# Kernel optimization log

Measured on AMD Instinct MI355X. Metric: run time of the kernel, lower is better.

Reference implementation:

```python
import jax, jax.numpy as jnp
import numpy as np

N = 20000          # nodes
E = 320000         # directed edges (self-loops added in reference)
F_IN = 128         # input node features
HEADS = 8
HID = 64           # per-head hidden channels
G = 64             # graphs in the batch
NUM_CLASSES = 10
NEG_SLOPE = 0.2    # PyG GATConv LeakyReLU slope


def _gat_layer(x, src, dst, W, a_src, a_dst, bias, n_nodes):
    """PyG-style GATConv: messages flow src->dst, softmax over incoming edges."""
    H, C = a_src.shape
    h = (x @ W).reshape(n_nodes, H, C)                     # [N,H,C]
    asrc = jnp.einsum('nhc,hc->nh', h, a_src)              # [N,H]
    adst = jnp.einsum('nhc,hc->nh', h, a_dst)              # [N,H]
    e = jax.nn.leaky_relu(asrc[src] + adst[dst], NEG_SLOPE)  # [Etot,H]
    emax = jax.ops.segment_max(e, dst, num_segments=n_nodes)  # [N,H]
    ee = jnp.exp(e - emax[dst])
    denom = jax.ops.segment_sum(ee, dst, num_segments=n_nodes)
    alpha = ee / (denom[dst] + 1e-16)                      # [Etot,H]
    out = jax.ops.segment_sum(h[src] * alpha[:, :, None], dst, num_segments=n_nodes)
    return out.reshape(n_nodes, H * C) + bias


def setup_inputs() -> dict:
    key = jax.random.key(0)
    ks = jax.random.split(key, 10)
    x = jax.random.normal(ks[0], (N, F_IN), jnp.float32)
    edge_index = jax.random.randint(ks[1], (2, E), 0, N, jnp.int32)
    batch = jnp.sort(jax.random.randint(ks[2], (N,), 0, G, jnp.int32))
    # layer 1: F_IN -> HEADS*HID (concat)
    W1 = jax.random.normal(ks[3], (F_IN, HEADS * HID), jnp.float32) / np.float32(np.sqrt(F_IN))
    a_src1 = jax.random.normal(ks[4], (HEADS, HID), jnp.float32) / np.float32(np.sqrt(HID))
    a_dst1 = jax.random.normal(ks[5], (HEADS, HID), jnp.float32) / np.float32(np.sqrt(HID))
    b1 = jnp.zeros((HEADS * HID,), jnp.float32)
    # layer 2: HEADS*HID -> NUM_CLASSES (1 head)
    W2 = jax.random.normal(ks[6], (HEADS * HID, NUM_CLASSES), jnp.float32) / np.float32(np.sqrt(HEADS * HID))
    a_src2 = jax.random.normal(ks[7], (1, NUM_CLASSES), jnp.float32) / np.float32(np.sqrt(NUM_CLASSES))
    a_dst2 = jax.random.normal(ks[8], (1, NUM_CLASSES), jnp.float32) / np.float32(np.sqrt(NUM_CLASSES))
    b2 = jnp.zeros((NUM_CLASSES,), jnp.float32)
    return {"x": x, "edge_index": edge_index, "batch": batch,
            "W1": W1, "a_src1": a_src1, "a_dst1": a_dst1, "b1": b1,
            "W2": W2, "a_src2": a_src2, "a_dst2": a_dst2, "b2": b2}


def reference(x, edge_index, batch, W1, a_src1, a_dst1, b1, W2, a_src2, a_dst2, b2):
    n = x.shape[0]
    loop = jnp.arange(n, dtype=edge_index.dtype)   # add_self_loops=True (PyG default)
    src = jnp.concatenate([edge_index[0], loop])
    dst = jnp.concatenate([edge_index[1], loop])
    h = jax.nn.elu(_gat_layer(x, src, dst, W1, a_src1, a_dst1, b1, n))
    h = _gat_layer(h, src, dst, W2, a_src2, a_dst2, b2, n)
    # PowerMeanAggregation with default p=1.0 == mean pooling per graph
    sums = jax.ops.segment_sum(h, batch, num_segments=G)                    # [G,NC]
    counts = jax.ops.segment_sum(jnp.ones((n, 1), h.dtype), batch, num_segments=G)
    return sums / jnp.maximum(counts, 1.0)
```

## Files before the change

kernel.cpp:

```cpp
#include <hip/hip_runtime.h>
#include <hip/hip_bf16.h>

typedef unsigned short ushort_t;
typedef unsigned int uint_t;
typedef unsigned char uchar_t;

typedef __attribute__((ext_vector_type(8))) short bf16x8;
typedef __attribute__((ext_vector_type(4))) float f32x4;
typedef __attribute__((ext_vector_type(2))) float f32x2;

__device__ __forceinline__ float bf2f(ushort_t u) {
    union { uint_t i; float f; } v; v.i = ((uint_t)u) << 16; return v.f;
}
__device__ __forceinline__ ushort_t f2bf(float f) {
    __hip_bfloat16 h = __float2bfloat16(f);
    ushort_t u; __builtin_memcpy(&u, &h, 2); return u;
}
__device__ __forceinline__ float leaky(float v) { return (v > 0.f) ? v : 0.2f * v; }

#define PO_AS1 0
#define PO_AD1 512
#define PO_B1  1024
#define PO_W2  1536
#define PO_AS2 6656
#define PO_AD2 6666
#define PO_B2  6676
#define PTOT   6686

__device__ __forceinline__ bool detect_fp32_local(const ushort_t* __restrict__ xa) {
    __shared__ int cnt;
    if (threadIdx.x == 0) cnt = 0;
    __syncthreads();
    int bad = 0;
    for (int i = threadIdx.x; i < 4096; i += 256) {
        float v = bf2f(xa[i]);
        if (!(fabsf(v) < 1e4f)) bad++;
    }
    if (bad) atomicAdd(&cnt, bad);
    __syncthreads();
    return cnt >= 16;
}

__global__ __launch_bounds__(256) void k_prep(const void* __restrict__ x,
                                              const void* __restrict__ W1,
                                              const void* as1, const void* ad1,
                                              const void* b1, const void* W2,
                                              const void* as2, const void* ad2,
                                              const void* b2,
                                              ushort_t* __restrict__ W1t,
                                              float* __restrict__ prm,
                                              float* __restrict__ vab,
                                              int* __restrict__ deg,
                                              float* __restrict__ gacc,
                                              int* __restrict__ flag, int N) {
    int b = blockIdx.x, t = threadIdx.x;
    if (b < 283) {
        bool isf = detect_fp32_local((const ushort_t*)x);
        if (b == 0 && t == 0) *flag = isf ? 1 : 0;
        if (b < 256) {
            int idx = b * 256 + t;
            int n = idx & 511, k = idx >> 9;
            float v = isf ? ((const float*)W1)[k * 512 + n]
                          : bf2f(((const ushort_t*)W1)[k * 512 + n]);
            W1t[n * 128 + k] = f2bf(v);
        } else {
            int i = (b - 256) * 256 + t;
            if (i < PTOT) {
                const void* src; int off;
                if (i < 512)       { src = as1; off = i; }
                else if (i < 1024) { src = ad1; off = i - 512; }
                else if (i < 1536) { src = b1;  off = i - 1024; }
                else if (i < 6656) { src = W2;  off = i - 1536; }
                else if (i < 6666) { src = as2; off = i - 6656; }
                else if (i < 6676) { src = ad2; off = i - 6666; }
                else               { src = b2;  off = i - 6676; }
                prm[i] = isf ? ((const float*)src)[off] : bf2f(((const ushort_t*)src)[off]);
            }
        }
    } else if (b < 362) {
        int i = (b - 283) * 256 + t;
        if (i < N) deg[i] = 0;
    } else if (b == 362) {
        for (int i = t; i < 704; i += 256) gacc[i] = 0.f;
    } else {
        bool isf = detect_fp32_local((const ushort_t*)x);
        int idx = (b - 363) * 256 + t;
        int k = idx >> 4, q = idx & 15;
        int h = q & 7;
        const void* av = (q < 8) ? as1 : ad1;
        float s = 0.f;
        for (int c = 0; c < 64; ++c) {
            float wv = isf ? ((const float*)W1)[k * 512 + h * 64 + c]
                           : bf2f(((const ushort_t*)W1)[k * 512 + h * 64 + c]);
            float aval = isf ? ((const float*)av)[h * 64 + c]
                             : bf2f(((const ushort_t*)av)[h * 64 + c]);
            s += wv * aval;
        }
        vab[k * 16 + q] = s;
    }
}

__global__ __launch_bounds__(256) void k_logits_hist(const void* __restrict__ xraw,
                                                     const float* __restrict__ vab,
                                                     const int* __restrict__ ei,
                                                     const int* __restrict__ flag,
                                                     uchar_t* __restrict__ xq,
                                                     float* __restrict__ asrcf,
                                                     float* __restrict__ adstf,
                                                     int* __restrict__ deg,
                                                     int E, int Etot) {
    int b = blockIdx.x, t = threadIdx.x;
    if (b >= 1250) {
        int e = (b - 1250) * 256 + t;
        if (e < Etot) {
            int dst = (e < E) ? ei[E + e] : (e - E);
            atomicAdd(&deg[dst], 1);
        }
        return;
    }
    bool isf = (*flag != 0);
    int n = b * 16 + (t >> 4);
    int l = t & 15;
    int ch0 = l * 8;
    float xf[8];
    if (isf) {
        const float4* x4 = (const float4*)xraw + (size_t)n * 32 + l * 2;
        float4 f0 = x4[0], f1 = x4[1];
        xf[0] = f0.x; xf[1] = f0.y; xf[2] = f0.z; xf[3] = f0.w;
        xf[4] = f1.x; xf[5] = f1.y; xf[6] = f1.z; xf[7] = f1.w;
    } else {
        uint4 u = ((const uint4*)((const ushort_t*)xraw + (size_t)n * 128))[l];
        xf[0] = bf2f(u.x & 0xffff); xf[1] = bf2f(u.x >> 16);
        xf[2] = bf2f(u.y & 0xffff); xf[3] = bf2f(u.y >> 16);
        xf[4] = bf2f(u.z & 0xffff); xf[5] = bf2f(u.z >> 16);
        xf[6] = bf2f(u.w & 0xffff); xf[7] = bf2f(u.w >> 16);
    }
    uint_t u0 = (uint_t)__builtin_amdgcn_cvt_pk_fp8_f32(xf[0], xf[1], 0, false);
    u0 = (uint_t)__builtin_amdgcn_cvt_pk_fp8_f32(xf[2], xf[3], (int)u0, true);
    uint_t u1 = (uint_t)__builtin_amdgcn_cvt_pk_fp8_f32(xf[4], xf[5], 0, false);
    u1 = (uint_t)__builtin_amdgcn_cvt_pk_fp8_f32(xf[6], xf[7], (int)u1, true);
    uint2 st; st.x = u0; st.y = u1;
    *((uint2*)(xq + (size_t)n * 128) + l) = st;
    float ps[8], pd[8];
#pragma unroll
    for (int h = 0; h < 8; ++h) { ps[h] = 0.f; pd[h] = 0.f; }
#pragma unroll
    for (int j = 0; j < 8; ++j) {
        const float4* vr = (const float4*)&vab[(ch0 + j) * 16];
        float4 va0 = vr[0], va1 = vr[1], vb0 = vr[2], vb1 = vr[3];
        float xv = xf[j];
        ps[0] += xv * va0.x; ps[1] += xv * va0.y; ps[2] += xv * va0.z; ps[3] += xv * va0.w;
        ps[4] += xv * va1.x; ps[5] += xv * va1.y; ps[6] += xv * va1.z; ps[7] += xv * va1.w;
        pd[0] += xv * vb0.x; pd[1] += xv * vb0.y; pd[2] += xv * vb0.z; pd[3] += xv * vb0.w;
        pd[4] += xv * vb1.x; pd[5] += xv * vb1.y; pd[6] += xv * vb1.z; pd[7] += xv * vb1.w;
    }
#pragma unroll
    for (int off = 1; off <= 8; off <<= 1) {
#pragma unroll
        for (int h = 0; h < 8; ++h) {
            ps[h] += __shfl_xor(ps[h], off, 64);
            pd[h] += __shfl_xor(pd[h], off, 64);
        }
    }
    if (l == 0) {
#pragma unroll
        for (int h = 0; h < 8; ++h) {
            asrcf[n * 8 + h] = ps[h];
            adstf[n * 8 + h] = pd[h];
        }
    }
}

__global__ __launch_bounds__(256) void k_scan(const int* __restrict__ deg,
                                              int* __restrict__ rowptr,
                                              int* __restrict__ cursor, int N) {
    int b = blockIdx.x, t = threadIdx.x;
    int lane = t & 63, wv = t >> 6;
    __shared__ int ws[4], wt[4];
    __shared__ int sbase;
    int limit = b * 256;
    int p0 = 0, p1 = 0, p2 = 0, p3 = 0;
    int i = t;
    for (; i + 768 < limit; i += 1024) {
        p0 += deg[i]; p1 += deg[i + 256]; p2 += deg[i + 512]; p3 += deg[i + 768];
    }
    for (; i < limit; i += 256) p0 += deg[i];
    int partial = (p0 + p1) + (p2 + p3);
#pragma unroll
    for (int off = 32; off; off >>= 1) partial += __shfl_xor(partial, off, 64);
    if (lane == 0) ws[wv] = partial;
    __syncthreads();
    if (t == 0) sbase = ws[0] + ws[1] + ws[2] + ws[3];
    __syncthreads();
    int base = sbase;
    i = limit + t;
    int v = (i < N) ? deg[i] : 0;
    int inc = v;
#pragma unroll
    for (int off = 1; off < 64; off <<= 1) {
        int u = __shfl_up(inc, off, 64);
        if (lane >= off) inc += u;
    }
    if (lane == 63) wt[wv] = inc;
    __syncthreads();
    int woff = 0;
    for (int w = 0; w < 4; ++w) if (w < wv) woff += wt[w];
    int excl = base + woff + inc - v;
    if (i < N) { rowptr[i + 1] = excl + v; cursor[i] = excl; }
    if (i == 0) rowptr[0] = 0;
}

__global__ __launch_bounds__(256) void k_scatter(const int* __restrict__ ei,
                                                 int* __restrict__ cursor,
                                                 const float* __restrict__ asrcf,
                                                 const float* __restrict__ adstf,
                                                 int* __restrict__ csr_src,
                                                 float* __restrict__ wcsr,
                                                 int E, int Etot) {
    int e = blockIdx.x * 256 + threadIdx.x;
    if (e >= Etot) return;
    int src, dst;
    if (e < E) { src = ei[e]; dst = ei[E + e]; } else { src = dst = e - E; }
    int pos = atomicAdd(&cursor[dst], 1);
    csr_src[pos] = src;
    const float4* ap = (const float4*)&asrcf[(size_t)src * 8];
    const float4* bp = (const float4*)&adstf[(size_t)dst * 8];
    float4 a0 = ap[0], a1 = ap[1];
    float4 b0 = bp[0], b1 = bp[1];
    float4 w0, w1;
    w0.x = __expf(leaky(a0.x + b0.x));
    w0.y = __expf(leaky(a0.y + b0.y));
    w0.z = __expf(leaky(a0.z + b0.z));
    w0.w = __expf(leaky(a0.w + b0.w));
    w1.x = __expf(leaky(a1.x + b1.x));
    w1.y = __expf(leaky(a1.y + b1.y));
    w1.z = __expf(leaky(a1.z + b1.z));
    w1.w = __expf(leaky(a1.w + b1.w));
    float4* wp = (float4*)&wcsr[(size_t)pos * 8];
    wp[0] = w0; wp[1] = w1;
}

__global__ __launch_bounds__(256) void k_aggx(const uchar_t* __restrict__ xq,
                                              const int* __restrict__ rowptr,
                                              const int* __restrict__ csr_src,
                                              const float* __restrict__ wcsr,
                                              ushort_t* __restrict__ agg) {
    int wid = threadIdx.x >> 6;
    int ni = wid >> 1;
    int half = wid & 1;
    int n = blockIdx.x * 2 + ni;
    int lane = threadIdx.x & 63;
    int start = rowptr[n], end = rowptr[n + 1];
    int deg = end - start;
    int mid = (deg + 1) >> 1;
    int es = start + (half ? mid : 0);
    int ee = half ? end : (start + mid);
    float acc[16];
    float den[8];
#pragma unroll
    for (int i = 0; i < 16; ++i) acc[i] = 0.f;
#pragma unroll
    for (int h = 0; h < 8; ++h) den[h] = 0.f;
    for (int base = es; base < ee; base += 64) {
        int m = min(64, ee - base);
        int sIdx = csr_src[base + min(lane, m - 1)];
        for (int g = 0; g < m; g += 4) {
            int s[4]; float4 wA[4], wB[4]; ushort_t xv[4];
#pragma unroll
            for (int j = 0; j < 4; ++j)
                s[j] = __shfl(sIdx, min(g + j, m - 1), 64);
#pragma unroll
            for (int j = 0; j < 4; ++j) {
                const float4* wp = (const float4*)&wcsr[(size_t)(base + g + j) * 8];
                wA[j] = wp[0]; wB[j] = wp[1];
            }
#pragma unroll
            for (int j = 0; j < 4; ++j)
                xv[j] = *(const ushort_t*)&xq[(size_t)s[j] * 128 + lane * 2];
#pragma unroll
            for (int j = 0; j < 4; ++j) {
                float msk = (g + j < m) ? 1.f : 0.f;
                f32x2 q = __builtin_amdgcn_cvt_pk_f32_fp8((int)xv[j], false);
                float w0 = wA[j].x * msk, w1 = wA[j].y * msk, w2 = wA[j].z * msk, w3 = wA[j].w * msk;
                float w4 = wB[j].x * msk, w5 = wB[j].y * msk, w6 = wB[j].z * msk, w7 = wB[j].w * msk;
                den[0] += w0; acc[0]  += w0 * q.x; acc[1]  += w0 * q.y;
                den[1] += w1; acc[2]  += w1 * q.x; acc[3]  += w1 * q.y;
                den[2] += w2; acc[4]  += w2 * q.x; acc[5]  += w2 * q.y;
                den[3] += w3; acc[6]  += w3 * q.x; acc[7]  += w3 * q.y;
                den[4] += w4; acc[8]  += w4 * q.x; acc[9]  += w4 * q.y;
                den[5] += w5; acc[10] += w5 * q.x; acc[11] += w5 * q.y;
                den[6] += w6; acc[12] += w6 * q.x; acc[13] += w6 * q.y;
                den[7] += w7; acc[14] += w7 * q.x; acc[15] += w7 * q.y;
            }
        }
    }
    __shared__ float sac[2][64][17];
    __shared__ float sdn[2][8];
    if (half) {
#pragma unroll
        for (int i = 0; i < 16; ++i) sac[ni][lane][i] = acc[i];
        if (lane == 0) {
#pragma unroll
            for (int h = 0; h < 8; ++h) sdn[ni][h] = den[h];
        }
    }
    __syncthreads();
    if (half) return;
#pragma unroll
    for (int i = 0; i < 16; ++i) acc[i] += sac[ni][lane][i];
    uint_t* arow = (uint_t*)&agg[(size_t)n * 1024];
#pragma unroll
    for (int h = 0; h < 8; ++h) {
        float inv = 1.f / (den[h] + sdn[ni][h] + 1e-16f);
        uint_t u = (uint_t)f2bf(acc[2 * h] * inv) | ((uint_t)f2bf(acc[2 * h + 1] * inv) << 16);
        arow[h * 64 + lane] = u;
    }
}

__global__ __launch_bounds__(256) void k_gemm2(const ushort_t* __restrict__ agg,
                                               const ushort_t* __restrict__ w1t,
                                               const float* __restrict__ prm,
                                               ushort_t* __restrict__ h2,
                                               float* __restrict__ asrc2f,
                                               float* __restrict__ adst2f) {
    __shared__ ushort_t sA[16 * 1040];
    int b = blockIdx.x, t = threadIdx.x;
    int m0 = b * 16;
    {
        const uint4* gsrc = (const uint4*)(agg + (size_t)m0 * 1024);
        for (int i = t; i < 2048; i += 256) {
            int row = i >> 7, part = i & 127;
            ((uint4*)sA)[row * 130 + part] = gsrc[i];
        }
    }
    __syncthreads();
    int wave = t >> 6, lane = t & 63;
    int mr = lane & 15, quad = lane >> 4;
    int n0 = wave * 128;
    f32x4 acc[8];
#pragma unroll
    for (int ct = 0; ct < 8; ++ct) acc[ct] = {0.f, 0.f, 0.f, 0.f};
#pragma unroll
    for (int kk = 0; kk < 4; ++kk) {
        bf16x8 a0 = *reinterpret_cast<const bf16x8*>(
            &sA[mr * 1040 + (wave * 2) * 128 + quad * 8 + kk * 32]);
        bf16x8 a1 = *reinterpret_cast<const bf16x8*>(
            &sA[mr * 1040 + (wave * 2 + 1) * 128 + quad * 8 + kk * 32]);
#pragma unroll
        for (int ct = 0; ct < 8; ++ct) {
            bf16x8 bb = *reinterpret_cast<const bf16x8*>(
                &w1t[(size_t)(n0 + ct * 16 + mr) * 128 + quad * 8 + kk * 32]);
            acc[ct] = __builtin_amdgcn_mfma_f32_16x16x32_bf16(ct < 4 ? a0 : a1, bb, acc[ct], 0, 0, 0);
        }
    }
    __syncthreads();
    ushort_t* h1s = sA;
    int col = lane & 15;
#pragma unroll
    for (int ct = 0; ct < 8; ++ct) {
        int abscol = n0 + ct * 16 + col;
        float bb1 = prm[PO_B1 + abscol];
#pragma unroll
        for (int r = 0; r < 4; ++r) {
            float v = acc[ct][r] + bb1;
            v = (v > 0.f) ? v : expm1f(v);
            h1s[(quad * 4 + r) * 512 + abscol] = f2bf(v);
        }
    }
    __syncthreads();
    int cb = lane * 8;
    for (int mm = 0; mm < 4; ++mm) {
        int m = wave * 4 + mm;
        int n = m0 + m;
        bf16x8 hv = *reinterpret_cast<const bf16x8*>(&h1s[m * 512 + cb]);
        float p2[10];
#pragma unroll
        for (int c = 0; c < 10; ++c) p2[c] = 0.f;
#pragma unroll
        for (int j = 0; j < 8; ++j) {
            float rv = bf2f((ushort_t)hv[j]);
            const float2* wrow = reinterpret_cast<const float2*>(&prm[PO_W2 + (cb + j) * 10]);
            float2 w01 = wrow[0], w23 = wrow[1], w45 = wrow[2], w67 = wrow[3], w89 = wrow[4];
            p2[0] += rv * w01.x; p2[1] += rv * w01.y;
            p2[2] += rv * w23.x; p2[3] += rv * w23.y;
            p2[4] += rv * w45.x; p2[5] += rv * w45.y;
            p2[6] += rv * w67.x; p2[7] += rv * w67.y;
            p2[8] += rv * w89.x; p2[9] += rv * w89.y;
        }
#pragma unroll
        for (int c = 0; c < 10; ++c)
#pragma unroll
            for (int off = 32; off; off >>= 1)
                p2[c] += __shfl_xor(p2[c], off, 64);
        if (lane == 0) {
            float as = 0.f, ad = 0.f;
#pragma unroll
            for (int c = 0; c < 10; ++c) {
                h2[(size_t)n * 16 + c] = f2bf(p2[c]);
                as += p2[c] * prm[PO_AS2 + c];
                ad += p2[c] * prm[PO_AD2 + c];
            }
            asrc2f[n] = as; adst2f[n] = ad;
        }
    }
}

__global__ __launch_bounds__(256) void k_agg2(const ushort_t* __restrict__ h2,
                                              const float* __restrict__ asrc2f,
                                              const float* __restrict__ adst2f,
                                              const int* __restrict__ rowptr,
                                              const int* __restrict__ csr_src,
                                              const float* __restrict__ prm,
                                              const int* __restrict__ batch,
                                              float* __restrict__ gacc,
                                              float* __restrict__ gcnt) {
    int t = threadIdx.x;
    int grp = t >> 4, l = t & 15;
    int n = blockIdx.x * 16 + grp;
    int start = rowptr[n], end = rowptr[n + 1];
    float adn = adst2f[n];
    float den = 0.f;
    float oc[10];
#pragma unroll
    for (int c = 0; c < 10; ++c) oc[c] = 0.f;
    for (int e = start + l; e < end; e += 16) {
        int s = csr_src[e];
        float lo = asrc2f[s];
        const uint_t* hp = (const uint_t*)(h2 + (size_t)s * 16);
        uint4 ha = *(const uint4*)hp;
        uint_t hb = hp[4];
        float ee = __expf(leaky(lo + adn));
        den += ee;
        oc[0] += ee * bf2f(ha.x & 0xffff); oc[1] += ee * bf2f(ha.x >> 16);
        oc[2] += ee * bf2f(ha.y & 0xffff); oc[3] += ee * bf2f(ha.y >> 16);
        oc[4] += ee * bf2f(ha.z & 0xffff); oc[5] += ee * bf2f(ha.z >> 16);
        oc[6] += ee * bf2f(ha.w & 0xffff); oc[7] += ee * bf2f(ha.w >> 16);
        oc[8] += ee * bf2f(hb & 0xffff);   oc[9] += ee * bf2f(hb >> 16);
    }
#pragma unroll
    for (int off = 8; off; off >>= 1) {
        den += __shfl_xor(den, off, 64);
#pragma unroll
        for (int c = 0; c < 10; ++c) oc[c] += __shfl_xor(oc[c], off, 64);
    }
    __shared__ float sres[16][12];
    __shared__ int sg[16];
    if (l == 0) {
        float invd = 1.f / (den + 1e-16f);
#pragma unroll
        for (int c = 0; c < 10; ++c) sres[grp][c] = oc[c] * invd + prm[PO_B2 + c];
        sres[grp][10] = 1.f;
        sg[grp] = batch[n];
    }
    __syncthreads();
    if (t < 11) {
        int c = t;
        float run = sres[0][c]; int g = sg[0];
        for (int k = 1; k < 16; ++k) {
            if (sg[k] != g) {
                atomicAdd(c < 10 ? &gacc[g * 10 + c] : &gcnt[g], run);
                g = sg[k]; run = 0.f;
            }
            run += sres[k][c];
        }
        atomicAdd(c < 10 ? &gacc[g * 10 + c] : &gcnt[g], run);
    }
}

__global__ void k_final(const float* __restrict__ gacc,
                        const float* __restrict__ gcnt,
                        const int* __restrict__ flag,
                        void* __restrict__ dout) {
    int g = threadIdx.x;
    if (g >= 64) return;
    bool isf = (*flag != 0);
    float cnt = fmaxf(gcnt[g], 1.f);
    for (int c = 0; c < 10; ++c) {
        float r = gacc[g * 10 + c] / cnt;
        if (isf) ((float*)dout)[g * 10 + c] = r;
        else     ((ushort_t*)dout)[g * 10 + c] = f2bf(r);
    }
}

extern "C" void kernel_launch(void* const* d_in, const int* in_sizes, int n_in,
                              void* d_out, int out_size, void* d_ws, size_t ws_size,
                              hipStream_t stream) {
    const void* x   = d_in[0];
    const int* ei   = (const int*)d_in[1];
    const int* batch= (const int*)d_in[2];
    const void* W1  = d_in[3];
    const void* as1 = d_in[4];
    const void* ad1 = d_in[5];
    const void* b1  = d_in[6];
    const void* W2  = d_in[7];
    const void* as2 = d_in[8];
    const void* ad2 = d_in[9];
    const void* b2  = d_in[10];

    constexpr int N = 20000, E = 320000, Etot = E + N;
    constexpr int histBlocks = (Etot + 255) / 256;

    char* p = (char*)d_ws;
    auto alloc = [&](size_t bytes) {
        char* r = p; p += (bytes + 255) & ~(size_t)255; return r;
    };
    int* flag       = (int*)alloc(256);
    float* prm      = (float*)alloc((size_t)PTOT * 4);
    float* vab      = (float*)alloc(2048 * 4);
    ushort_t* w1t   = (ushort_t*)alloc(512 * 128 * 2);
    uchar_t* xq     = (uchar_t*)alloc((size_t)N * 128);
    float* asrc1f   = (float*)alloc((size_t)N * 8 * 4);
    float* adst1f   = (float*)alloc((size_t)N * 8 * 4);
    float* asrc2f   = (float*)alloc((size_t)N * 4);
    float* adst2f   = (float*)alloc((size_t)N * 4);
    ushort_t* h2    = (ushort_t*)alloc((size_t)N * 16 * 2);
    float* gacc     = (float*)alloc((size_t)(64 * 10 + 64) * 4);
    int* deg        = (int*)alloc((size_t)N * 4);
    int* rowptr     = (int*)alloc((size_t)(N + 1) * 4);
    int* cursor     = (int*)alloc((size_t)N * 4);
    int* csr_src    = (int*)alloc((size_t)(Etot + 64) * 4);
    float* wcsr     = (float*)alloc(((size_t)Etot * 8 + 128) * 4);
    ushort_t* agg   = (ushort_t*)alloc((size_t)N * 1024 * 2);
    float* gcnt     = gacc + 640;

    k_prep<<<371, 256, 0, stream>>>(x, W1, as1, ad1, b1, W2, as2, ad2, b2,
                                    w1t, prm, vab, deg, gacc, flag, N);
    k_logits_hist<<<1250 + histBlocks, 256, 0, stream>>>(x, vab, ei, flag, xq,
                                                         asrc1f, adst1f, deg, E, Etot);
    k_scan<<<(N + 255) / 256, 256, 0, stream>>>(deg, rowptr, cursor, N);
    k_scatter<<<histBlocks, 256, 0, stream>>>(ei, cursor, asrc1f, adst1f,
                                              csr_src, wcsr, E, Etot);
    k_aggx<<<N / 2, 256, 0, stream>>>(xq, rowptr, csr_src, wcsr, agg);
    k_gemm2<<<1250, 256, 0, stream>>>(agg, w1t, prm, h2, asrc2f, adst2f);
    k_agg2<<<N / 16, 256, 0, stream>>>(h2, asrc2f, adst2f, rowptr, csr_src, prm,
                                       batch, gacc, gcnt);
    k_final<<<1, 64, 0, stream>>>(gacc, gcnt, flag, d_out);
}
```

Baseline: 256.6 us.

## Fuse layer-1 aggregation into GEMM kernel and fold final mean into agg2

The layer-1 neighbor aggregation now writes each block's 16 aggregated rows straight into shared memory and feeds the MFMA GEMM directly. This removes the global bf16 agg buffer (20000x1024) and one kernel launch. The final mean-pooling kernel is folded into agg2 using a last-block-done atomic counter. The trade-off is less aggregation parallelism: one wave handles 4 nodes serially with no split-half reduction, and 1250 blocks replace 10000, so latency hiding for the gather may be worse.

```diff
diff --git a/kernel.cpp b/kernel.cpp
--- a/kernel.cpp
+++ b/kernel.cpp
@@ -81,7 +81,7 @@
         int i = (b - 283) * 256 + t;
         if (i < N) deg[i] = 0;
     } else if (b == 362) {
-        for (int i = t; i < 704; i += 256) gacc[i] = 0.f;
+        for (int i = t; i < 768; i += 256) gacc[i] = 0.f;
     } else {
         bool isf = detect_fp32_local((const ushort_t*)x);
         int idx = (b - 363) * 256 + t;
@@ -240,106 +240,75 @@
     wp[0] = w0; wp[1] = w1;
 }
 
-__global__ __launch_bounds__(256) void k_aggx(const uchar_t* __restrict__ xq,
-                                              const int* __restrict__ rowptr,
-                                              const int* __restrict__ csr_src,
-                                              const float* __restrict__ wcsr,
-                                              ushort_t* __restrict__ agg) {
-    int wid = threadIdx.x >> 6;
-    int ni = wid >> 1;
-    int half = wid & 1;
-    int n = blockIdx.x * 2 + ni;
-    int lane = threadIdx.x & 63;
-    int start = rowptr[n], end = rowptr[n + 1];
-    int deg = end - start;
-    int mid = (deg + 1) >> 1;
-    int es = start + (half ? mid : 0);
-    int ee = half ? end : (start + mid);
-    float acc[16];
-    float den[8];
-#pragma unroll
-    for (int i = 0; i < 16; ++i) acc[i] = 0.f;
-#pragma unroll
-    for (int h = 0; h < 8; ++h) den[h] = 0.f;
-    for (int base = es; base < ee; base += 64) {
-        int m = min(64, ee - base);
-        int sIdx = csr_src[base + min(lane, m - 1)];
-        for (int g = 0; g < m; g += 4) {
-            int s[4]; float4 wA[4], wB[4]; ushort_t xv[4];
-#pragma unroll
-            for (int j = 0; j < 4; ++j)
-                s[j] = __shfl(sIdx, min(g + j, m - 1), 64);
-#pragma unroll
-            for (int j = 0; j < 4; ++j) {
-                const float4* wp = (const float4*)&wcsr[(size_t)(base + g + j) * 8];
-                wA[j] = wp[0]; wB[j] = wp[1];
-            }
-#pragma unroll
-            for (int j = 0; j < 4; ++j)
-                xv[j] = *(const ushort_t*)&xq[(size_t)s[j] * 128 + lane * 2];
-#pragma unroll
-            for (int j = 0; j < 4; ++j) {
-                float msk = (g + j < m) ? 1.f : 0.f;
-                f32x2 q = __builtin_amdgcn_cvt_pk_f32_fp8((int)xv[j], false);
-                float w0 = wA[j].x * msk, w1 = wA[j].y * msk, w2 = wA[j].z * msk, w3 = wA[j].w * msk;
-                float w4 = wB[j].x * msk, w5 = wB[j].y * msk, w6 = wB[j].z * msk, w7 = wB[j].w * msk;
-                den[0] += w0; acc[0]  += w0 * q.x; acc[1]  += w0 * q.y;
-                den[1] += w1; acc[2]  += w1 * q.x; acc[3]  += w1 * q.y;
-                den[2] += w2; acc[4]  += w2 * q.x; acc[5]  += w2 * q.y;
-                den[3] += w3; acc[6]  += w3 * q.x; acc[7]  += w3 * q.y;
-                den[4] += w4; acc[8]  += w4 * q.x; acc[9]  += w4 * q.y;
-                den[5] += w5; acc[10] += w5 * q.x; acc[11] += w5 * q.y;
-                den[6] += w6; acc[12] += w6 * q.x; acc[13] += w6 * q.y;
-                den[7] += w7; acc[14] += w7 * q.x; acc[15] += w7 * q.y;
-            }
-        }
-    }
-    __shared__ float sac[2][64][17];
-    __shared__ float sdn[2][8];
-    if (half) {
-#pragma unroll
-        for (int i = 0; i < 16; ++i) sac[ni][lane][i] = acc[i];
-        if (lane == 0) {
-#pragma unroll
-            for (int h = 0; h < 8; ++h) sdn[ni][h] = den[h];
-        }
-    }
-    __syncthreads();
-    if (half) return;
-#pragma unroll
-    for (int i = 0; i < 16; ++i) acc[i] += sac[ni][lane][i];
-    uint_t* arow = (uint_t*)&agg[(size_t)n * 1024];
-#pragma unroll
-    for (int h = 0; h < 8; ++h) {
-        float inv = 1.f / (den[h] + sdn[ni][h] + 1e-16f);
-        uint_t u = (uint_t)f2bf(acc[2 * h] * inv) | ((uint_t)f2bf(acc[2 * h + 1] * inv) << 16);
-        arow[h * 64 + lane] = u;
-    }
-}
-
-__global__ __launch_bounds__(256) void k_gemm2(const ushort_t* __restrict__ agg,
-                                               const ushort_t* __restrict__ w1t,
-                                               const float* __restrict__ prm,
-                                               ushort_t* __restrict__ h2,
-                                               float* __restrict__ asrc2f,
-                                               float* __restrict__ adst2f) {
+__global__ __launch_bounds__(256) void k_aggfused(const uchar_t* __restrict__ xq,
+                                                  const int* __restrict__ rowptr,
+                                                  const int* __restrict__ csr_src,
+                                                  const float* __restrict__ wcsr,
+                                                  const ushort_t* __restrict__ w1t,
+                                                  const float* __restrict__ prm,
+                                                  ushort_t* __restrict__ h2,
+                                                  float* __restrict__ asrc2f,
+                                                  float* __restrict__ adst2f) {
     __shared__ ushort_t sA[16 * 1040];
     int b = blockIdx.x, t = threadIdx.x;
     int m0 = b * 16;
-    {
-        const uint4* gsrc = (const uint4*)(agg + (size_t)m0 * 1024);
-        for (int i = t; i < 2048; i += 256) {
-            int row = i >> 7, part = i & 127;
-            ((uint4*)sA)[row * 130 + part] = gsrc[i];
-        }
-    }
-    __syncthreads();
     int wave = t >> 6, lane = t & 63;
+    for (int mm = 0; mm < 4; ++mm) {
+        int mloc = wave * 4 + mm;
+        int n = m0 + mloc;
+        int start = rowptr[n], end = rowptr[n + 1];
+        float acc[16];
+        float den[8];
+#pragma unroll
+        for (int i = 0; i < 16; ++i) acc[i] = 0.f;
+#pragma unroll
+        for (int h = 0; h < 8; ++h) den[h] = 0.f;
+        for (int base = start; base < end; base += 64) {
+            int mcap = min(64, end - base);
+            int sIdx = csr_src[base + min(lane, mcap - 1)];
+            for (int g = 0; g < mcap; g += 4) {
+                int s[4]; float4 wA[4], wB[4]; ushort_t xv[4];
+#pragma unroll
+                for (int j = 0; j < 4; ++j)
+                    s[j] = __shfl(sIdx, min(g + j, mcap - 1), 64);
+#pragma unroll
+                for (int j = 0; j < 4; ++j) {
+                    const float4* wp = (const float4*)&wcsr[(size_t)(base + min(g + j, mcap - 1)) * 8];
+                    wA[j] = wp[0]; wB[j] = wp[1];
+                }
+#pragma unroll
+                for (int j = 0; j < 4; ++j)
+                    xv[j] = *(const ushort_t*)&xq[(size_t)s[j] * 128 + lane * 2];
+#pragma unroll
+                for (int j = 0; j < 4; ++j) {
+                    float msk = (g + j < mcap) ? 1.f : 0.f;
+                    f32x2 q = __builtin_amdgcn_cvt_pk_f32_fp8((int)xv[j], false);
+                    float w0 = wA[j].x * msk, w1 = wA[j].y * msk, w2 = wA[j].z * msk, w3 = wA[j].w * msk;
+                    float w4 = wB[j].x * msk, w5 = wB[j].y * msk, w6 = wB[j].z * msk, w7 = wB[j].w * msk;
+                    den[0] += w0; acc[0]  += w0 * q.x; acc[1]  += w0 * q.y;
+                    den[1] += w1; acc[2]  += w1 * q.x; acc[3]  += w1 * q.y;
+                    den[2] += w2; acc[4]  += w2 * q.x; acc[5]  += w2 * q.y;
+                    den[3] += w3; acc[6]  += w3 * q.x; acc[7]  += w3 * q.y;
+                    den[4] += w4; acc[8]  += w4 * q.x; acc[9]  += w4 * q.y;
+                    den[5] += w5; acc[10] += w5 * q.x; acc[11] += w5 * q.y;
+                    den[6] += w6; acc[12] += w6 * q.x; acc[13] += w6 * q.y;
+                    den[7] += w7; acc[14] += w7 * q.x; acc[15] += w7 * q.y;
+                }
+            }
+        }
+#pragma unroll
+        for (int h = 0; h < 8; ++h) {
+            float inv = 1.f / (den[h] + 1e-16f);
+            uint_t u = (uint_t)f2bf(acc[2 * h] * inv) | ((uint_t)f2bf(acc[2 * h + 1] * inv) << 16);
+            *(uint_t*)&sA[mloc * 1040 + h * 128 + 2 * lane] = u;
+        }
+    }
+    __syncthreads();
     int mr = lane & 15, quad = lane >> 4;
     int n0 = wave * 128;
-    f32x4 acc[8];
-#pragma unroll
-    for (int ct = 0; ct < 8; ++ct) acc[ct] = {0.f, 0.f, 0.f, 0.f};
+    f32x4 acc2[8];
+#pragma unroll
+    for (int ct = 0; ct < 8; ++ct) acc2[ct] = {0.f, 0.f, 0.f, 0.f};
 #pragma unroll
     for (int kk = 0; kk < 4; ++kk) {
         bf16x8 a0 = *reinterpret_cast<const bf16x8*>(
@@ -350,7 +319,7 @@
         for (int ct = 0; ct < 8; ++ct) {
             bf16x8 bb = *reinterpret_cast<const bf16x8*>(
                 &w1t[(size_t)(n0 + ct * 16 + mr) * 128 + quad * 8 + kk * 32]);
-            acc[ct] = __builtin_amdgcn_mfma_f32_16x16x32_bf16(ct < 4 ? a0 : a1, bb, acc[ct], 0, 0, 0);
+            acc2[ct] = __builtin_amdgcn_mfma_f32_16x16x32_bf16(ct < 4 ? a0 : a1, bb, acc2[ct], 0, 0, 0);
         }
     }
     __syncthreads();
@@ -362,7 +331,7 @@
         float bb1 = prm[PO_B1 + abscol];
 #pragma unroll
         for (int r = 0; r < 4; ++r) {
-            float v = acc[ct][r] + bb1;
+            float v = acc2[ct][r] + bb1;
             v = (v > 0.f) ? v : expm1f(v);
             h1s[(quad * 4 + r) * 512 + abscol] = f2bf(v);
         }
@@ -405,15 +374,18 @@
     }
 }
 
-__global__ __launch_bounds__(256) void k_agg2(const ushort_t* __restrict__ h2,
-                                              const float* __restrict__ asrc2f,
-                                              const float* __restrict__ adst2f,
-                                              const int* __restrict__ rowptr,
-                                              const int* __restrict__ csr_src,
-                                              const float* __restrict__ prm,
-                                              const int* __restrict__ batch,
-                                              float* __restrict__ gacc,
-                                              float* __restrict__ gcnt) {
+__global__ __launch_bounds__(256) void k_agg2f(const ushort_t* __restrict__ h2,
+                                               const float* __restrict__ asrc2f,
+                                               const float* __restrict__ adst2f,
+                                               const int* __restrict__ rowptr,
+                                               const int* __restrict__ csr_src,
+                                               const float* __restrict__ prm,
+                                               const int* __restrict__ batch,
+                                               float* __restrict__ gacc,
+                                               float* __restrict__ gcnt,
+                                               int* __restrict__ donecnt,
+                                               const int* __restrict__ flag,
+                                               void* __restrict__ dout) {
     int t = threadIdx.x;
     int grp = t >> 4, l = t & 15;
     int n = blockIdx.x * 16 + grp;
@@ -465,20 +437,25 @@
         }
         atomicAdd(c < 10 ? &gacc[g * 10 + c] : &gcnt[g], run);
     }
-}
-
-__global__ void k_final(const float* __restrict__ gacc,
-                        const float* __restrict__ gcnt,
-                        const int* __restrict__ flag,
-                        void* __restrict__ dout) {
-    int g = threadIdx.x;
-    if (g >= 64) return;
-    bool isf = (*flag != 0);
-    float cnt = fmaxf(gcnt[g], 1.f);
-    for (int c = 0; c < 10; ++c) {
-        float r = gacc[g * 10 + c] / cnt;
-        if (isf) ((float*)dout)[g * 10 + c] = r;
-        else     ((ushort_t*)dout)[g * 10 + c] = f2bf(r);
+    __syncthreads();
+    __shared__ int slast;
+    if (t == 0) {
+        __threadfence();
+        int d = atomicAdd(donecnt, 1);
+        slast = (d == (int)gridDim.x - 1) ? 1 : 0;
+    }
+    __syncthreads();
+    if (slast && t < 64) {
+        __threadfence();
+        bool isf = (*flag != 0);
+        const volatile float* ga = (const volatile float*)gacc;
+        const volatile float* gc = (const volatile float*)gcnt;
+        float cnt = fmaxf(gc[t], 1.f);
+        for (int c = 0; c < 10; ++c) {
+            float r = ga[t * 10 + c] / cnt;
+            if (isf) ((float*)dout)[t * 10 + c] = r;
+            else     ((ushort_t*)dout)[t * 10 + c] = f2bf(r);
+        }
     }
 }
 
@@ -514,14 +491,14 @@
     float* asrc2f   = (float*)alloc((size_t)N * 4);
     float* adst2f   = (float*)alloc((size_t)N * 4);
     ushort_t* h2    = (ushort_t*)alloc((size_t)N * 16 * 2);
-    float* gacc     = (float*)alloc((size_t)(64 * 10 + 64) * 4);
+    float* gacc     = (float*)alloc((size_t)768 * 4);
     int* deg        = (int*)alloc((size_t)N * 4);
     int* rowptr     = (int*)alloc((size_t)(N + 1) * 4);
     int* cursor     = (int*)alloc((size_t)N * 4);
     int* csr_src    = (int*)alloc((size_t)(Etot + 64) * 4);
-    float* wcsr     = (float*)alloc(((size_t)Etot * 8 + 128) * 4);
-    ushort_t* agg   = (ushort_t*)alloc((size_t)N * 1024 * 2);
+    float* wcsr     = (float*)alloc(((size_t)Etot * 8 + 1024) * 4);
     float* gcnt     = gacc + 640;
+    int* donecnt    = (int*)(gacc + 704);
 
     k_prep<<<371, 256, 0, stream>>>(x, W1, as1, ad1, b1, W2, as2, ad2, b2,
                                     w1t, prm, vab, deg, gacc, flag, N);
@@ -530,9 +507,8 @@
     k_scan<<<(N + 255) / 256, 256, 0, stream>>>(deg, rowptr, cursor, N);
     k_scatter<<<histBlocks, 256, 0, stream>>>(ei, cursor, asrc1f, adst1f,
                                               csr_src, wcsr, E, Etot);
-    k_aggx<<<N / 2, 256, 0, stream>>>(xq, rowptr, csr_src, wcsr, agg);
-    k_gemm2<<<1250, 256, 0, stream>>>(agg, w1t, prm, h2, asrc2f, adst2f);
-    k_agg2<<<N / 16, 256, 0, stream>>>(h2, asrc2f, adst2f, rowptr, csr_src, prm,
-                                       batch, gacc, gcnt);
-    k_final<<<1, 64, 0, stream>>>(gacc, gcnt, flag, d_out);
-}
+    k_aggfused<<<1250, 256, 0, stream>>>(xq, rowptr, csr_src, wcsr, w1t, prm,
+                                         h2, asrc2f, adst2f);
+    k_agg2f<<<N / 16, 256, 0, stream>>>(h2, asrc2f, adst2f, rowptr, csr_src, prm,
+                                        batch, gacc, gcnt, donecnt, flag, d_out);
+}
```

Result: no change. 257.7 us (+0.4%).
